# Kernel tuning notes

Hardware: AMD Instinct MI355X
Metric: run time of the kernel (lower is better)

Reference implementation:

```python
import jax, jax.numpy as jnp
import numpy as np

BATCH = 4096      # batch_size (number of graphs)
TOTAL = 1048576   # total atoms across the batch
D = 128           # feature dim


def setup_inputs() -> dict:
    key = jax.random.key(0)
    k1, k2 = jax.random.split(key)
    atom_features = jax.random.normal(k1, (TOTAL, D), dtype=jnp.float32)
    molecule_indicator = jnp.sort(jax.random.randint(k2, (TOTAL,), 0, BATCH)).astype(jnp.int64)
    return {"atom_features": atom_features, "molecule_indicator": molecule_indicator}


def reference(atom_features, molecule_indicator):
    # Ragged -> padded conversion as a single fused scatter instead of a
    # Python loop of O(batch_size) boolean-mask gathers + pads + stack.
    total, d = atom_features.shape
    mi = molecule_indicator.astype(jnp.int32)
    # atoms per graph
    counts = jax.ops.segment_sum(jnp.ones((total,), jnp.int32), mi, num_segments=BATCH)
    # intra-graph position of each atom (indicator is sorted / contiguous per graph)
    starts = jnp.cumsum(counts) - counts            # exclusive prefix sum [BATCH]
    pos = jnp.arange(total, dtype=jnp.int32) - starts[mi]
    # data-dependent padded length, matching torch's max(num_atoms)
    max_num_atoms = int(jnp.max(counts))
    padded = jnp.zeros((BATCH, max_num_atoms, d), atom_features.dtype)
    padded = padded.at[mi, pos].set(atom_features)  # [BATCH, max_atoms, D]
    # original: keep graphs whose padded block does not sum to exactly 0
    # (i.e. drop empty graphs). Data-dependent gather, evaluated eagerly.
    block_sums = jnp.sum(padded, axis=(1, 2))
    keep = np.nonzero(np.asarray(block_sums != 0))[0]
    return padded[keep]
```

## Files before the change

kernel.cpp:

```cpp
#include <hip/hip_runtime.h>

#define BATCH 4096
#define D 128

typedef float floatx4 __attribute__((ext_vector_type(4)));


__global__ void detect_dtype_kernel(const int* __restrict__ mi, int total, int* __restrict__ ws) {
    if (threadIdx.x == 0 && blockIdx.x == 0) {
        ws[4102] = (mi[total - 1] == 0) ? 1 : 0;
    }
}

__global__ void compute_starts_kernel(const int* __restrict__ mi, int total, int* __restrict__ ws) {
    int t = blockIdx.x * blockDim.x + threadIdx.x;
    if (t > BATCH) return;
    const int is64 = ws[4102];
    int lo = 0, hi = total;
    while (lo < hi) {
        int mid = (lo + hi) >> 1;
        int v = is64 ? mi[(long long)mid << 1] : mi[mid];
        if (v < t) lo = mid + 1; else hi = mid;
    }
    ws[t] = lo;
}

__global__ __launch_bounds__(1024) void compute_meta_kernel(int* __restrict__ ws) {
    const int* starts = ws;
    int* kept = ws + 4104;
    __shared__ int smax[1024];
    __shared__ int ssum[1024];
    const int tid = threadIdx.x;

    int cnt4[4];
    int localmax = 0;
    int localkeep = 0;
#pragma unroll
    for (int j = 0; j < 4; ++j) {
        int b = tid * 4 + j;
        int c = starts[b + 1] - starts[b];
        cnt4[j] = c;
        localmax = max(localmax, c);
        localkeep += (c > 0) ? 1 : 0;
    }
    smax[tid] = localmax;
    ssum[tid] = localkeep;
    __syncthreads();

    for (int s = 512; s > 0; s >>= 1) {
        if (tid < s) smax[tid] = max(smax[tid], smax[tid + s]);
        __syncthreads();
    }
    for (int off = 1; off < 1024; off <<= 1) {
        int v = (tid >= off) ? ssum[tid - off] : 0;
        __syncthreads();
        ssum[tid] += v;
        __syncthreads();
    }
    int excl = ssum[tid] - localkeep;
    int o = excl;
#pragma unroll
    for (int j = 0; j < 4; ++j) {
        int b = tid * 4 + j;
        if (cnt4[j] > 0) kept[o++] = b;
    }
    if (tid == 0)    ws[4100] = smax[0];
    if (tid == 1023) ws[4101] = ssum[1023];
}

__global__ __launch_bounds__(256) void fill_out_kernel(const floatx4* __restrict__ in4,
                                                       const int* __restrict__ ws,
                                                       floatx4* __restrict__ out4,
                                                       int n4) {
    const int* starts = ws;
    const int* kept = ws + 4104;
    const int max_atoms = ws[4100];

    int idx = blockIdx.x * blockDim.x + threadIdx.x;
    const int stride = gridDim.x * blockDim.x;
    for (; idx < n4; idx += stride) {
        int r = idx >> 5;
        int c = idx & 31;
        int g = r / max_atoms;
        int row = r - g * max_atoms;
        int b = kept[g];
        int s = starts[b];
        int cnt = starts[b + 1] - s;
        floatx4 v = (floatx4)(0.f);
        if (row < cnt) {
            v = in4[((s + row) << 5) + c];
        }
        __builtin_nontemporal_store(v, &out4[idx]);
    }
}

extern "C" void kernel_launch(void* const* d_in, const int* in_sizes, int n_in,
                              void* d_out, int out_size, void* d_ws, size_t ws_size,
                              hipStream_t stream) {
    const float* feat = (const float*)d_in[0];
    const int* mi = (const int*)d_in[1];
    const int total = in_sizes[1];
    float* out = (float*)d_out;
    int* ws = (int*)d_ws;

    detect_dtype_kernel<<<1, 64, 0, stream>>>(mi, total, ws);
    compute_starts_kernel<<<(BATCH + 1 + 255) / 256, 256, 0, stream>>>(mi, total, ws);
    compute_meta_kernel<<<1, 1024, 0, stream>>>(ws);

    const int n4 = out_size / 4;
    fill_out_kernel<<<4096, 256, 0, stream>>>((const floatx4*)feat, ws, (floatx4*)out, n4);
}
```

Measured before the change: 250.6 us.

## Copy padded output per graph with split blocks instead of flat grid-stride fill

Replaces the flat grid-stride fill kernel, which did an integer division and metadata lookups for every vector element, with a kernel that assigns each kept graph to SPLIT blocks. Each block copies the graph's valid rows with nontemporal loads and stores, then writes zeros for the padding rows. This removes per-element division and index lookups and lets the copy and zero phases run branch-free. Load balance now depends on graph sizes, and blocks for dropped graph slots exit immediately.

```diff
diff --git a/kernel.cpp b/kernel.cpp
--- a/kernel.cpp
+++ b/kernel.cpp
@@ -2,6 +2,7 @@
 
 #define BATCH 4096
 #define D 128
+#define SPLIT 4
 
 typedef float floatx4 __attribute__((ext_vector_type(4)));
 
@@ -68,29 +69,34 @@
     if (tid == 1023) ws[4101] = ssum[1023];
 }
 
-__global__ __launch_bounds__(256) void fill_out_kernel(const floatx4* __restrict__ in4,
-                                                       const int* __restrict__ ws,
-                                                       floatx4* __restrict__ out4,
-                                                       int n4) {
-    const int* starts = ws;
-    const int* kept = ws + 4104;
+__global__ __launch_bounds__(256) void copy_graph_kernel(const floatx4* __restrict__ in4,
+                                                         const int* __restrict__ ws,
+                                                         floatx4* __restrict__ out4) {
+    const int g = blockIdx.x / SPLIT;
+    const int p = blockIdx.x - g * SPLIT;
+    const int keep_count = ws[4101];
+    if (g >= keep_count) return;
+
+    const int b = ws[4104 + g];
+    const int s = ws[b];
+    const int cnt = ws[b + 1] - s;
     const int max_atoms = ws[4100];
 
-    int idx = blockIdx.x * blockDim.x + threadIdx.x;
-    const int stride = gridDim.x * blockDim.x;
-    for (; idx < n4; idx += stride) {
-        int r = idx >> 5;
-        int c = idx & 31;
-        int g = r / max_atoms;
-        int row = r - g * max_atoms;
-        int b = kept[g];
-        int s = starts[b];
-        int cnt = starts[b + 1] - s;
-        floatx4 v = (floatx4)(0.f);
-        if (row < cnt) {
-            v = in4[((s + row) << 5) + c];
-        }
-        __builtin_nontemporal_store(v, &out4[idx]);
+    const floatx4* __restrict__ src = in4 + (s << 5);
+    floatx4* __restrict__ dst = out4 + (g * max_atoms << 5);
+    const int ncopy = cnt << 5;
+    const int ntot = max_atoms << 5;
+
+    int i = threadIdx.x + (p << 8);
+    const int stride = 256 * SPLIT;
+
+#pragma unroll 4
+    for (; i < ncopy; i += stride) {
+        __builtin_nontemporal_store(__builtin_nontemporal_load(&src[i]), &dst[i]);
+    }
+#pragma unroll 4
+    for (; i < ntot; i += stride) {
+        __builtin_nontemporal_store((floatx4)(0.f), &dst[i]);
     }
 }
 
@@ -107,6 +113,5 @@
     compute_starts_kernel<<<(BATCH + 1 + 255) / 256, 256, 0, stream>>>(mi, total, ws);
     compute_meta_kernel<<<1, 1024, 0, stream>>>(ws);
 
-    const int n4 = out_size / 4;
-    fill_out_kernel<<<4096, 256, 0, stream>>>((const floatx4*)feat, ws, (floatx4*)out, n4);
+    copy_graph_kernel<<<BATCH * SPLIT, 256, 0, stream>>>((const floatx4*)feat, ws, (floatx4*)out);
 }
```

After: 223.2 us. -10.9%, faster.
